# Kernel tuning notes

Measured on AMD Instinct MI355X. Metric: run time of the kernel, lower is better.

The kernel has to match this reference:

```python
import jax, jax.numpy as jnp
import numpy as np

KS = 3            # kernel_size per axis
K3 = KS * KS * KS  # 27 flattened kernel bins
_OFFSETS = np.array([[dz, dy, dx] for dz in (0, 1) for dy in (0, 1) for dx in (0, 1)], np.int32)  # 8 trilinear corners
_STRIDES = np.array([KS * KS, KS, 1], np.int32)
EPS = 1e-12


def continuous_conv(features, pos_input, pos_output, extents, kernel, bias):
    """Open3D-style ContinuousConv: ball_to_cube_radial mapping, poly6 window,
    trilinear kernel interpolation, per-output-point weighted aggregate."""
    No, Ni = pos_output.shape[0], pos_input.shape[0]
    # normalized relative positions: unit ball of radius extents/2 -> r in [0,1)
    rel = (pos_input[None, :, :] - pos_output[:, None, :]) * (2.0 / extents[0])  # [No,Ni,3]
    r2 = jnp.sum(rel * rel, axis=-1)                                             # [No,Ni]
    inside = r2 < 1.0
    window = jnp.where(inside, (1.0 - r2) ** 3, 0.0)        # poly6 window, zero outside support
    r = jnp.sqrt(jnp.maximum(r2, EPS))
    linf = jnp.max(jnp.abs(rel), axis=-1)
    # radial ball->cube map: scale each point by ||p||_2 / ||p||_inf
    scale = jnp.where(linf > EPS, r / jnp.maximum(linf, EPS), 1.0)
    q = jnp.clip(rel * scale[..., None], -1.0, 1.0)         # cube coords in [-1,1]^3
    t = (q + 1.0) * 0.5 * (KS - 1)                          # grid coords in [0, KS-1]
    t0 = jnp.clip(jnp.floor(t), 0, KS - 2).astype(jnp.int32)
    f = t - t0                                              # trilinear fractions [No,Ni,3]
    off = jnp.asarray(_OFFSETS)                             # [8,3]
    cw = jnp.where(off[None, None, :, :] == 1, f[:, :, None, :], 1.0 - f[:, :, None, :])
    w8 = cw.prod(axis=-1) * window[:, :, None]              # [No,Ni,8] corner weights
    idx8 = jnp.sum((t0[:, :, None, :] + off) * jnp.asarray(_STRIDES), axis=-1)  # [No,Ni,8] flat bin
    ii = jnp.arange(No)[:, None, None]
    jj = jnp.arange(Ni)[None, :, None]
    # A[i,j,k]: interpolation weight of input j into kernel bin k for output i
    A = jnp.zeros((No, Ni, K3), features.dtype).at[ii, jj, idx8].add(w8)
    B = jnp.einsum('ijk,jc->ikc', A, features)              # aggregate features per bin
    out = jnp.einsum('ikc,kcf->if', B, kernel) + bias       # contract with learned kernel
    return out


def setup_inputs() -> dict:
    key = jax.random.key(0)
    k1, k2, k3, k4 = jax.random.split(key, 4)
    N_IN, N_OUT, C_IN, C_OUT = 2048, 2048, 8, 64
    features = jax.random.normal(k1, (N_IN, C_IN), dtype=jnp.float32)
    pos_input = jax.random.uniform(k2, (N_IN, 3), dtype=jnp.float32)
    pos_output = jax.random.uniform(k3, (N_OUT, 3), dtype=jnp.float32)
    extents = jnp.ones((1,), dtype=jnp.float32)
    kernel = jax.random.normal(k4, (K3, C_IN, C_OUT), dtype=jnp.float32) * 0.05
    bias = jnp.zeros((C_OUT,), dtype=jnp.float32)
    return {"features": features, "pos_input": pos_input, "pos_output": pos_output,
            "extents": extents, "kernel": kernel, "bias": bias}


def reference(features, pos_input, pos_output, extents, kernel, bias):
    x = continuous_conv(features, pos_input, pos_output, extents, kernel, bias)
    return jax.nn.relu(x)
```

## Files before the change

### kernel.cpp

```cpp
#include <hip/hip_runtime.h>

#define KS 3
#define K3 27
#define CIN 8
#define COUT 64
#define CC_EPS 1e-12f
#define LIST_CAP 1024

__global__ __launch_bounds__(256)
void cconv_fused_kernel(const float* __restrict__ features,
                        const float* __restrict__ pos_input,
                        const float* __restrict__ pos_output,
                        const float* __restrict__ extents,
                        const float* __restrict__ kern,
                        const float* __restrict__ bias,
                        float* __restrict__ out,
                        int Ni, int No)
{
    const int tid  = threadIdx.x;
    const int wave = tid >> 6;
    const int lane = tid & 63;
    const int p    = wave >> 1;
    const int half = wave & 1;
    const int i    = blockIdx.x * 2 + p;

    __shared__ unsigned short idx[4][LIST_CAP];
    __shared__ float Bsh[4][K3][CIN];
    __shared__ float part[4][COUT];

    const bool activeI = (i < No);

    float ox = 0.f, oy = 0.f, oz = 0.f, s = 1.f;
    if (activeI) {
        s  = 2.0f / extents[0];
        ox = pos_output[i * 3 + 0];
        oy = pos_output[i * 3 + 1];
        oz = pos_output[i * 3 + 2];
    }

    const int jbeg = half ? (Ni >> 1) : 0;
    const int jend = half ? Ni : (Ni >> 1);
    int cnt = 0;
    if (activeI) {
        for (int j0 = jbeg; j0 < jend; j0 += 64) {
            const int j = j0 + lane;
            bool inside = false;
            if (j < jend) {
                const float rx = (pos_input[j * 3 + 0] - ox) * s;
                const float ry = (pos_input[j * 3 + 1] - oy) * s;
                const float rz = (pos_input[j * 3 + 2] - oz) * s;
                inside = (rx * rx + ry * ry + rz * rz) < 1.0f;
            }
            const unsigned long long m = __ballot(inside);
            if (inside) {
                const int pre = __popcll(m & ((1ull << lane) - 1ull));
                idx[wave][cnt + pre] = (unsigned short)j;
            }
            cnt += (int)__popcll(m);
        }
    }

    float acc[K3];
#pragma unroll
    for (int k = 0; k < K3; ++k) acc[k] = 0.0f;

    if (activeI && cnt > 0) {
        const int jsub = lane >> 3;
        const int c    = lane & 7;
        for (int it = 0; it < cnt; it += 8) {
            const int  slot  = it + jsub;
            const bool valid = (slot < cnt);
            const int  j     = idx[wave][valid ? slot : (cnt - 1)];

            const float rx = (pos_input[j * 3 + 0] - ox) * s;
            const float ry = (pos_input[j * 3 + 1] - oy) * s;
            const float rz = (pos_input[j * 3 + 2] - oz) * s;
            const float fval = valid ? features[j * CIN + c] : 0.0f;

            const float r2  = rx * rx + ry * ry + rz * rz;
            const float u   = 1.0f - r2;
            const float win = u * u * u;
            const float r   = sqrtf(fmaxf(r2, CC_EPS));
            const float linf = fmaxf(fmaxf(fabsf(rx), fabsf(ry)), fabsf(rz));
            const float scale = (linf > CC_EPS) ? (r / linf) : 1.0f;
            const float ta = fminf(fmaxf(rx * scale, -1.f), 1.f) + 1.0f;
            const float tb = fminf(fmaxf(ry * scale, -1.f), 1.f) + 1.0f;
            const float tc = fminf(fmaxf(rz * scale, -1.f), 1.f) + 1.0f;
            const float wa0 = fmaxf(1.0f - ta, 0.0f), wa2 = fmaxf(ta - 1.0f, 0.0f);
            const float wb0 = fmaxf(1.0f - tb, 0.0f), wb2 = fmaxf(tb - 1.0f, 0.0f);
            const float wc0 = fmaxf(1.0f - tc, 0.0f), wc2 = fmaxf(tc - 1.0f, 0.0f);
            const float wa1 = 1.0f - wa0 - wa2;
            const float wb1 = 1.0f - wb0 - wb2;
            const float wc1 = 1.0f - wc0 - wc2;

            const float wav[3] = { wa0 * win,  wa1 * win,  wa2 * win  };
            const float wbv[3] = { wb0,        wb1,        wb2        };
            const float wcf[3] = { wc0 * fval, wc1 * fval, wc2 * fval };
#pragma unroll
            for (int a = 0; a < 3; ++a) {
#pragma unroll
                for (int b = 0; b < 3; ++b) {
                    const float wab = wav[a] * wbv[b];
#pragma unroll
                    for (int c3 = 0; c3 < 3; ++c3) {
                        acc[a * 9 + b * 3 + c3] =
                            fmaf(wab, wcf[c3], acc[a * 9 + b * 3 + c3]);
                    }
                }
            }
        }
    }

#pragma unroll
    for (int k = 0; k < K3; ++k) {
        float v = acc[k];
        v += __shfl_xor(v, 8, 64);
        v += __shfl_xor(v, 16, 64);
        v += __shfl_xor(v, 32, 64);
        acc[k] = v;
    }
    if ((lane >> 3) == 0) {
        const int c = lane & 7;
#pragma unroll
        for (int k = 0; k < K3; ++k) Bsh[wave][k][c] = acc[k];
    }

    __syncthreads();

    {
        const int kb = half ? 14 : 0;
        const int ke = half ? K3 : 14;
        const int f  = lane;
        float o = 0.0f;
        for (int k = kb; k < ke; ++k) {
#pragma unroll
            for (int cc = 0; cc < CIN; ++cc) {
                const float b = Bsh[2 * p][k][cc] + Bsh[2 * p + 1][k][cc];
                o = fmaf(b, kern[(k * CIN + cc) * COUT + f], o);
            }
        }
        part[wave][f] = o;
    }
    __syncthreads();

    if (tid < 128) {
        const int pp = tid >> 6;
        const int f  = tid & 63;
        const int ii = blockIdx.x * 2 + pp;
        if (ii < No) {
            const float o = bias[f] + part[2 * pp][f] + part[2 * pp + 1][f];
            out[ii * COUT + f] = fmaxf(o, 0.0f);
        }
    }
}

extern "C" void kernel_launch(void* const* d_in, const int* in_sizes, int n_in,
                              void* d_out, int out_size, void* d_ws, size_t ws_size,
                              hipStream_t stream) {
    const float* features   = (const float*)d_in[0];
    const float* pos_input  = (const float*)d_in[1];
    const float* pos_output = (const float*)d_in[2];
    const float* extents    = (const float*)d_in[3];
    const float* kern       = (const float*)d_in[4];
    const float* bias       = (const float*)d_in[5];
    float* out = (float*)d_out;

    const int Ni = in_sizes[0] / CIN;
    const int No = in_sizes[2] / 3;

    dim3 block(256);
    dim3 grid((No + 1) / 2);
    cconv_fused_kernel<<<grid, block, 0, stream>>>(features, pos_input, pos_output,
                                                   extents, kern, bias, out, Ni, No);
}
```

Before: 117.9 us.

## Assign one output point per block with four waves sharing a compacted neighbor list

Each block now handles a single output point instead of two. All four waves scan interleaved input chunks and append in-ball indices to one shared list through an LDS atomic counter. The aggregation then spreads neighbors across all four waves, with a cross-wave reduction of the per-bin sums before the kernel contraction. The grid doubles, and fast hardware sqrt/rcp builtins replace the precise versions, which may slightly change numerics; neighbor order becomes nondeterministic, so floating-point summation order can vary between runs.

```diff
diff --git a/kernel.cpp b/kernel.cpp
--- a/kernel.cpp
+++ b/kernel.cpp
@@ -1,11 +1,10 @@
 #include <hip/hip_runtime.h>
 
-#define KS 3
 #define K3 27
 #define CIN 8
 #define COUT 64
 #define CC_EPS 1e-12f
-#define LIST_CAP 1024
+#define NI_CAP 2048
 
 __global__ __launch_bounds__(256)
 void cconv_fused_kernel(const float* __restrict__ features,
@@ -18,94 +17,90 @@
                         int Ni, int No)
 {
     const int tid  = threadIdx.x;
-    const int wave = tid >> 6;
+    const int w    = tid >> 6;
     const int lane = tid & 63;
-    const int p    = wave >> 1;
-    const int half = wave & 1;
-    const int i    = blockIdx.x * 2 + p;
+    const int i    = blockIdx.x;
 
-    __shared__ unsigned short idx[4][LIST_CAP];
+    __shared__ unsigned short idx[NI_CAP];
+    __shared__ int   cnt_sh;
     __shared__ float Bsh[4][K3][CIN];
+    __shared__ float Bf[K3][CIN];
     __shared__ float part[4][COUT];
 
-    const bool activeI = (i < No);
+    if (tid == 0) cnt_sh = 0;
+    __syncthreads();
 
-    float ox = 0.f, oy = 0.f, oz = 0.f, s = 1.f;
-    if (activeI) {
-        s  = 2.0f / extents[0];
-        ox = pos_output[i * 3 + 0];
-        oy = pos_output[i * 3 + 1];
-        oz = pos_output[i * 3 + 2];
-    }
+    const float s  = 2.0f / extents[0];
+    const float ox = pos_output[i * 3 + 0];
+    const float oy = pos_output[i * 3 + 1];
+    const float oz = pos_output[i * 3 + 2];
 
-    const int jbeg = half ? (Ni >> 1) : 0;
-    const int jend = half ? Ni : (Ni >> 1);
-    int cnt = 0;
-    if (activeI) {
-        for (int j0 = jbeg; j0 < jend; j0 += 64) {
-            const int j = j0 + lane;
-            bool inside = false;
-            if (j < jend) {
-                const float rx = (pos_input[j * 3 + 0] - ox) * s;
-                const float ry = (pos_input[j * 3 + 1] - oy) * s;
-                const float rz = (pos_input[j * 3 + 2] - oz) * s;
-                inside = (rx * rx + ry * ry + rz * rz) < 1.0f;
-            }
-            const unsigned long long m = __ballot(inside);
-            if (inside) {
-                const int pre = __popcll(m & ((1ull << lane) - 1ull));
-                idx[wave][cnt + pre] = (unsigned short)j;
-            }
-            cnt += (int)__popcll(m);
+    for (int j0 = w * 64; j0 < Ni; j0 += 256) {
+        const int j = j0 + lane;
+        bool inside = false;
+        if (j < Ni) {
+            const float rx = (pos_input[j * 3 + 0] - ox) * s;
+            const float ry = (pos_input[j * 3 + 1] - oy) * s;
+            const float rz = (pos_input[j * 3 + 2] - oz) * s;
+            inside = (rx * rx + ry * ry + rz * rz) < 1.0f;
+        }
+        const unsigned long long m = __ballot(inside);
+        const int nin = (int)__popcll(m);
+        int base = 0;
+        if (lane == 0 && nin) base = atomicAdd(&cnt_sh, nin);
+        base = __shfl(base, 0, 64);
+        if (inside) {
+            const int pre = __popcll(m & ((1ull << lane) - 1ull));
+            idx[base + pre] = (unsigned short)j;
         }
     }
+    __syncthreads();
+    const int total = cnt_sh;
 
     float acc[K3];
 #pragma unroll
     for (int k = 0; k < K3; ++k) acc[k] = 0.0f;
 
-    if (activeI && cnt > 0) {
-        const int jsub = lane >> 3;
-        const int c    = lane & 7;
-        for (int it = 0; it < cnt; it += 8) {
-            const int  slot  = it + jsub;
-            const bool valid = (slot < cnt);
-            const int  j     = idx[wave][valid ? slot : (cnt - 1)];
+    const int jsub = lane >> 3;
+    const int c    = lane & 7;
+    for (int base = w * 8; base < total; base += 32) {
+        const int  slot  = base + jsub;
+        const bool valid = (slot < total);
+        const int  j     = idx[valid ? slot : total - 1];
 
-            const float rx = (pos_input[j * 3 + 0] - ox) * s;
-            const float ry = (pos_input[j * 3 + 1] - oy) * s;
-            const float rz = (pos_input[j * 3 + 2] - oz) * s;
-            const float fval = valid ? features[j * CIN + c] : 0.0f;
+        const float rx = (pos_input[j * 3 + 0] - ox) * s;
+        const float ry = (pos_input[j * 3 + 1] - oy) * s;
+        const float rz = (pos_input[j * 3 + 2] - oz) * s;
+        const float fval = valid ? features[j * CIN + c] : 0.0f;
 
-            const float r2  = rx * rx + ry * ry + rz * rz;
-            const float u   = 1.0f - r2;
-            const float win = u * u * u;
-            const float r   = sqrtf(fmaxf(r2, CC_EPS));
-            const float linf = fmaxf(fmaxf(fabsf(rx), fabsf(ry)), fabsf(rz));
-            const float scale = (linf > CC_EPS) ? (r / linf) : 1.0f;
-            const float ta = fminf(fmaxf(rx * scale, -1.f), 1.f) + 1.0f;
-            const float tb = fminf(fmaxf(ry * scale, -1.f), 1.f) + 1.0f;
-            const float tc = fminf(fmaxf(rz * scale, -1.f), 1.f) + 1.0f;
-            const float wa0 = fmaxf(1.0f - ta, 0.0f), wa2 = fmaxf(ta - 1.0f, 0.0f);
-            const float wb0 = fmaxf(1.0f - tb, 0.0f), wb2 = fmaxf(tb - 1.0f, 0.0f);
-            const float wc0 = fmaxf(1.0f - tc, 0.0f), wc2 = fmaxf(tc - 1.0f, 0.0f);
-            const float wa1 = 1.0f - wa0 - wa2;
-            const float wb1 = 1.0f - wb0 - wb2;
-            const float wc1 = 1.0f - wc0 - wc2;
+        const float r2  = rx * rx + ry * ry + rz * rz;
+        const float u   = 1.0f - r2;
+        const float win = u * u * u;
+        const float r    = __builtin_amdgcn_sqrtf(fmaxf(r2, CC_EPS));
+        const float linf = fmaxf(fmaxf(fabsf(rx), fabsf(ry)), fabsf(rz));
+        const float scale = (linf > CC_EPS) ? r * __builtin_amdgcn_rcpf(linf) : 1.0f;
+        const float ta = fminf(fmaxf(rx * scale, -1.f), 1.f) + 1.0f;
+        const float tb = fminf(fmaxf(ry * scale, -1.f), 1.f) + 1.0f;
+        const float tc = fminf(fmaxf(rz * scale, -1.f), 1.f) + 1.0f;
+        const float wa0 = fmaxf(1.0f - ta, 0.0f), wa2 = fmaxf(ta - 1.0f, 0.0f);
+        const float wb0 = fmaxf(1.0f - tb, 0.0f), wb2 = fmaxf(tb - 1.0f, 0.0f);
+        const float wc0 = fmaxf(1.0f - tc, 0.0f), wc2 = fmaxf(tc - 1.0f, 0.0f);
+        const float wa1 = 1.0f - wa0 - wa2;
+        const float wb1 = 1.0f - wb0 - wb2;
+        const float wc1 = 1.0f - wc0 - wc2;
 
-            const float wav[3] = { wa0 * win,  wa1 * win,  wa2 * win  };
-            const float wbv[3] = { wb0,        wb1,        wb2        };
-            const float wcf[3] = { wc0 * fval, wc1 * fval, wc2 * fval };
+        const float wav[3] = { wa0 * win,  wa1 * win,  wa2 * win  };
+        const float wbv[3] = { wb0,        wb1,        wb2        };
+        const float wcf[3] = { wc0 * fval, wc1 * fval, wc2 * fval };
 #pragma unroll
-            for (int a = 0; a < 3; ++a) {
+        for (int a = 0; a < 3; ++a) {
 #pragma unroll
-                for (int b = 0; b < 3; ++b) {
-                    const float wab = wav[a] * wbv[b];
+            for (int b = 0; b < 3; ++b) {
+                const float wab = wav[a] * wbv[b];
 #pragma unroll
-                    for (int c3 = 0; c3 < 3; ++c3) {
-                        acc[a * 9 + b * 3 + c3] =
-                            fmaf(wab, wcf[c3], acc[a * 9 + b * 3 + c3]);
-                    }
+                for (int c3 = 0; c3 < 3; ++c3) {
+                    acc[a * 9 + b * 3 + c3] =
+                        fmaf(wab, wcf[c3], acc[a * 9 + b * 3 + c3]);
                 }
             }
         }
@@ -119,38 +114,38 @@
         v += __shfl_xor(v, 32, 64);
         acc[k] = v;
     }
-    if ((lane >> 3) == 0) {
-        const int c = lane & 7;
+    if (jsub == 0) {
 #pragma unroll
-        for (int k = 0; k < K3; ++k) Bsh[wave][k][c] = acc[k];
+        for (int k = 0; k < K3; ++k) Bsh[w][k][c] = acc[k];
     }
+    __syncthreads();
 
+    if (tid < K3 * CIN) {
+        const int k  = tid >> 3;
+        const int cc = tid & 7;
+        Bf[k][cc] = Bsh[0][k][cc] + Bsh[1][k][cc] + Bsh[2][k][cc] + Bsh[3][k][cc];
+    }
     __syncthreads();
 
     {
-        const int kb = half ? 14 : 0;
-        const int ke = half ? K3 : 14;
+        const int kb = w * 7;
+        const int ke = (kb + 7 < K3) ? kb + 7 : K3;
         const int f  = lane;
         float o = 0.0f;
         for (int k = kb; k < ke; ++k) {
 #pragma unroll
             for (int cc = 0; cc < CIN; ++cc) {
-                const float b = Bsh[2 * p][k][cc] + Bsh[2 * p + 1][k][cc];
-                o = fmaf(b, kern[(k * CIN + cc) * COUT + f], o);
+                o = fmaf(Bf[k][cc], kern[(k * CIN + cc) * COUT + f], o);
             }
         }
-        part[wave][f] = o;
+        part[w][f] = o;
     }
     __syncthreads();
 
-    if (tid < 128) {
-        const int pp = tid >> 6;
-        const int f  = tid & 63;
-        const int ii = blockIdx.x * 2 + pp;
-        if (ii < No) {
-            const float o = bias[f] + part[2 * pp][f] + part[2 * pp + 1][f];
-            out[ii * COUT + f] = fmaxf(o, 0.0f);
-        }
+    if (tid < COUT) {
+        const float o = bias[tid] + part[0][tid] + part[1][tid]
+                                  + part[2][tid] + part[3][tid];
+        out[i * COUT + tid] = fmaxf(o, 0.0f);
     }
 }
 
@@ -169,7 +164,7 @@
     const int No = in_sizes[2] / 3;
 
     dim3 block(256);
-    dim3 grid((No + 1) / 2);
+    dim3 grid(No);
     cconv_fused_kernel<<<grid, block, 0, stream>>>(features, pos_input, pos_output,
                                                    extents, kern, bias, out, Ni, No);
 }
```

Result: faster. 98.72 us (-16.3%).
